# Kernel tuning notes

Hardware: AMD Instinct MI355X
Metric: run time of the kernel (lower is better)

Reference implementation:

```python
import jax, jax.numpy as jnp
import numpy as np

CHEB_K = 2  # hops per support; stacked terms = 1 + 2*CHEB_K = 5


def setup_inputs() -> dict:
    key = jax.random.key(0)
    k1, k2, k3, k4, k5 = jax.random.split(key, 5)
    B, N, C, O, D = 16, 1024, 64, 64, 10
    return {
        "x": jax.random.normal(k1, (B, N, C), dtype=jnp.float32),
        "adj": jax.random.uniform(k2, (2, B, N, N), dtype=jnp.float32),
        "node_embedding": jax.random.normal(k3, (N, D), dtype=jnp.float32),
        "weights_pool": jax.random.normal(k4, (D, 2 * CHEB_K + 1, C, O), dtype=jnp.float32) * 0.1,
        "bias_pool": jax.random.normal(k5, (D, O), dtype=jnp.float32) * 0.1,
    }


def reference(x, adj, node_embedding, weights_pool, bias_pool):
    # k-hop graph aggregation over each of the 2 supports
    out = [x]
    for s in range(adj.shape[0]):
        a = adj[s]  # [B, N, N]
        x1 = x
        for _ in range(CHEB_K):
            x1 = jnp.einsum('bnm,bmc->bnc', a, x1)
            out.append(x1)
    x_g = jnp.stack(out, axis=2)  # [B, N, K, C] with K = 2*cheb_k+1 (already node-major)
    # per-node hypernetwork weights and bias from node embeddings
    weights = jnp.einsum('nd,dkio->nkio', node_embedding, weights_pool)  # [N, K, C, O]
    bias = node_embedding @ bias_pool  # [N, O]
    # per-node contraction over (K, C)
    return jnp.einsum('bnki,nkio->bno', x_g, weights) + bias
```

## Files before the change

### kernel.cpp

```cpp
#include <hip/hip_runtime.h>
#include <stdint.h>


typedef __attribute__((ext_vector_type(4))) float f32x4;
typedef __attribute__((ext_vector_type(8))) short s16x8;
typedef __attribute__((ext_vector_type(8))) __bf16 bf16x8;

__device__ __forceinline__ unsigned short f2bf(float f) {
  union { float f; uint32_t u; } v; v.f = f;
  uint32_t r = v.u + 0x7FFFu + ((v.u >> 16) & 1u);
  return (unsigned short)(r >> 16);
}
__device__ __forceinline__ uint32_t pack2(float a, float b) {
  return (uint32_t)f2bf(a) | ((uint32_t)f2bf(b) << 16);
}

union FragU { s16x8 s; bf16x8 b; uint32_t u[4]; };

__device__ __forceinline__ void async_cp16(const void* g, void* l) {
  __builtin_amdgcn_global_load_lds(
      (const __attribute__((address_space(1))) void*)g,
      (__attribute__((address_space(3))) void*)l, 16, 0, 0);
}

__global__ __launch_bounds__(256) void cvt_adj(const float* __restrict__ adj,
                                               unsigned short* __restrict__ adjb) {
  const size_t stride = (size_t)gridDim.x * 256 * 8;
  for (size_t p = ((size_t)blockIdx.x * 256 + threadIdx.x) * 8;
       p < 33554432u; p += stride) {
    f32x4 a = *(const f32x4*)(adj + p);
    f32x4 b = *(const f32x4*)(adj + p + 4);
    union { s16x8 s; uint32_t u[4]; } o;
    o.u[0] = pack2(a[0], a[1]);
    o.u[1] = pack2(a[2], a[3]);
    o.u[2] = pack2(b[0], b[1]);
    o.u[3] = pack2(b[2], b[3]);
    *(s16x8*)(adjb + p) = o.s;
  }
}

__global__ __launch_bounds__(256) void prep(const float* __restrict__ x,
                                            const float* __restrict__ wp,
                                            unsigned short* __restrict__ XT0,
                                            unsigned short* __restrict__ X0b,
                                            unsigned short* __restrict__ wpTb) {
  __shared__ __align__(16) char smem[17160];
  const int tid = threadIdx.x;
  const int bid = blockIdx.x;
  if (bid < 256) {
    unsigned short (*tl)[72] = (unsigned short(*)[72])smem;
    const int b = bid >> 4, n0 = (bid & 15) * 64;
    {
      const int c4 = (tid & 15) * 4;
#pragma unroll
      for (int i = 0; i < 4; ++i) {
        const int row = (tid >> 4) + i * 16;
        f32x4 v =
            *(const f32x4*)(x + ((size_t)(b * 1024 + n0 + row)) * 64 + c4);
        const uint32_t w0 = pack2(v[0], v[1]);
        const uint32_t w1 = pack2(v[2], v[3]);
        *(uint32_t*)&tl[row][c4]     = w0;
        *(uint32_t*)&tl[row][c4 + 2] = w1;
        const uint64_t wq = (uint64_t)w0 | ((uint64_t)w1 << 32);
        *(uint64_t*)(X0b + ((size_t)(b * 1024 + n0 + row)) * 64 + c4) = wq;
      }
    }
    __syncthreads();
    {
      const int c = tid >> 2;
      const int nch = (tid & 3) * 16;
      s16x8 s0, s1;
#pragma unroll
      for (int j = 0; j < 8; ++j) {
        s0[j] = (short)tl[nch + j][c];
        s1[j] = (short)tl[nch + 8 + j][c];
      }
      unsigned short* p = XT0 + (size_t)(b * 64 + c) * 1024 + n0 + nch;
      *(s16x8*)p = s0;
      *(s16x8*)(p + 8) = s1;
    }
  } else {
    float (*tl)[65] = (float(*)[65])smem;
    const int jj = bid - 256;
    const int d = jj / 5, ki0 = (jj % 5) * 64;
    const float* src = wp + (size_t)d * 20480;
    {
      const int o4 = (tid & 15) * 4;
#pragma unroll
      for (int i = 0; i < 4; ++i) {
        const int row = (tid >> 4) + i * 16;
        f32x4 v = *(const f32x4*)(src + (size_t)(ki0 + row) * 64 + o4);
        tl[row][o4] = v[0]; tl[row][o4 + 1] = v[1];
        tl[row][o4 + 2] = v[2]; tl[row][o4 + 3] = v[3];
      }
    }
    __syncthreads();
    {
      const int o = tid >> 2;
      const int kch = (tid & 3) * 16;
      s16x8 s0, s1;
#pragma unroll
      for (int j = 0; j < 8; ++j) {
        s0[j] = (short)f2bf(tl[kch + j][o]);
        s1[j] = (short)f2bf(tl[kch + 8 + j][o]);
      }
      const int c0 = (ki0 + kch) >> 3;
      unsigned short* base = wpTb + (size_t)d * 24576 + (size_t)o * 384;
      *(s16x8*)(base + ((c0) ^ (o & 7)) * 8) = s0;
      *(s16x8*)(base + ((c0 + 1) ^ (o & 7)) * 8) = s1;
    }
  }
}

__device__ __forceinline__ void hop_body(
    char* smem, const unsigned short* __restrict__ A,
    const unsigned short* __restrict__ XT, unsigned short* __restrict__ Xoutb,
    unsigned short* __restrict__ XTout, int write_xt, int rowbase) {
  const int tid = threadIdx.x;
  const int wave = tid >> 6, lane = tid & 63;
  const int l15 = lane & 15, q = lane >> 4;

  unsigned short* const Ast = (unsigned short*)smem;
  unsigned short* const Bst = (unsigned short*)smem + 8192;

  const int sub = lane >> 3;
  const int ch = lane & 7;
  const unsigned short* asrc[2];
  const unsigned short* bsrc[2];
  int ldso[2];
#pragma unroll
  for (int i = 0; i < 2; ++i) {
    const int r = wave * 16 + i * 8 + sub;
    asrc[i] = A + (size_t)(rowbase + r) * 1024 + (ch ^ (r & 7)) * 8;
    bsrc[i] = XT + (size_t)r * 1024 + (ch ^ (r & 7)) * 8;
    ldso[i] = (wave * 16 + i * 8) * 64;
  }

  f32x4 acc[4];
#pragma unroll
  for (int t = 0; t < 4; ++t) acc[t] = (f32x4){0.f, 0.f, 0.f, 0.f};

  auto issue = [&](int s, int k0) {
#pragma unroll
    for (int i = 0; i < 2; ++i) {
      async_cp16(asrc[i] + k0, Ast + s * 4096 + ldso[i]);
      async_cp16(bsrc[i] + k0, Bst + s * 4096 + ldso[i]);
    }
  };
  const int sw = l15 & 7;
  auto compute = [&](int s) {
    const unsigned short* Ab = Ast + s * 4096 + (wave * 16 + l15) * 64;
    const unsigned short* Bb = Bst + s * 4096 + l15 * 64;
#pragma unroll
    for (int h = 0; h < 2; ++h) {
      const int cko = ((h * 4 + q) ^ sw) * 8;
      FragU af;
      af.s = *(const s16x8*)(Ab + cko);
#pragma unroll
      for (int t = 0; t < 4; ++t) {
        FragU bf;
        bf.s = *(const s16x8*)(Bb + t * 1024 + cko);
        acc[t] = __builtin_amdgcn_mfma_f32_16x16x32_bf16(af.b, bf.b, acc[t],
                                                         0, 0, 0);
      }
    }
  };

  issue(0, 0);
#pragma unroll 1
  for (int kt = 0; kt < 16; ++kt) {
    const int cur = kt & 1;
    __syncthreads();
    if (kt + 1 < 16) issue(cur ^ 1, (kt + 1) * 64);
    compute(cur);
  }

  __syncthreads();
  float (*tile)[65] = (float(*)[65])smem;
#pragma unroll
  for (int t = 0; t < 4; ++t)
#pragma unroll
    for (int rr = 0; rr < 4; ++rr)
      tile[wave * 16 + q * 4 + rr][t * 16 + l15] = acc[t][rr];
  __syncthreads();

  {
    const int row = tid >> 2;
    const int cb = (tid & 3) * 16;
    unsigned short* __restrict__ outp =
        Xoutb + (size_t)(rowbase + row) * 64 + cb;
    s16x8 s0, s1;
#pragma unroll
    for (int j = 0; j < 8; ++j) {
      s0[j] = (short)f2bf(tile[row][cb + j]);
      s1[j] = (short)f2bf(tile[row][cb + 8 + j]);
    }
    *(s16x8*)outp = s0;
    *(s16x8*)(outp + 8) = s1;
  }
  if (write_xt) {
    const int c = tid >> 2;
    const int nch = (tid & 3) * 16;
    unsigned short* __restrict__ xtp = XTout + (size_t)c * 1024 + rowbase + nch;
    s16x8 s0, s1;
#pragma unroll
    for (int j = 0; j < 8; ++j) {
      s0[j] = (short)f2bf(tile[nch + j][c]);
      s1[j] = (short)f2bf(tile[nch + 8 + j][c]);
    }
    *(s16x8*)xtp = s0;
    *(s16x8*)(xtp + 8) = s1;
  }
}

__global__ __launch_bounds__(256, 4) void hop1_kernel(
    const unsigned short* __restrict__ adjb,
    const unsigned short* __restrict__ XT0, unsigned short* __restrict__ X1b,
    unsigned short* __restrict__ XT1) {
  __shared__ __align__(16) char smem[32768];
  const int bx = blockIdx.x, slice = blockIdx.y, b = slice & 15;
  hop_body(smem, adjb + (size_t)slice * 1048576, XT0 + (size_t)b * 65536,
           X1b + (size_t)slice * 65536, XT1 + (size_t)slice * 65536, 1,
           bx * 64);
}

__global__ __launch_bounds__(256, 4) void hop2_kernel(
    const unsigned short* __restrict__ adjb,
    const unsigned short* __restrict__ XT1, unsigned short* __restrict__ X2b) {
  __shared__ __align__(16) char smem[32768];
  const int bx = 15 - (int)blockIdx.x;
  const int slice = 31 - (int)blockIdx.y;
  hop_body(smem, adjb + (size_t)slice * 1048576, XT1 + (size_t)slice * 65536,
           X2b + (size_t)slice * 65536, (unsigned short*)0, 0, bx * 64);
}

__global__ __launch_bounds__(512, 4) void final_kernel(
    const unsigned short* __restrict__ X0b,
    const unsigned short* __restrict__ X1b,
    const unsigned short* __restrict__ X2b,
    const unsigned short* __restrict__ wpTb, const float* __restrict__ emb,
    const float* __restrict__ bp, float* __restrict__ out) {
  __shared__ __align__(16) unsigned short wd[64][384];
  const int tid = threadIdx.x, bid = blockIdx.x;
  const int wave = tid >> 6, lane = tid & 63;
  const int l15 = lane & 15, q = lane >> 4;
  const int nd = wave >> 1, oh = wave & 1;
  const int n = bid * 4 + nd;
  const int sw2 = l15 & 7;

  FragU af10[10];
#pragma unroll
  for (int ks = 0; ks < 10; ++ks) {
    const int k = ks >> 1;
    const int cc0 = (ks & 1) * 32 + q * 8;
    const unsigned short* srcp;
    if (k == 0) {
      srcp = X0b + ((size_t)l15 * 1024 + n) * 64 + cc0;
    } else {
      const unsigned short* arr = (k == 1 || k == 3) ? X1b : X2b;
      const int s = (k >= 3) ? 1 : 0;
      srcp = arr + ((size_t)(s * 16 + l15) * 1024 + n) * 64 + cc0;
    }
    af10[ks].s = *(const s16x8*)srcp;
  }

  f32x4 acc0 = {0.f, 0.f, 0.f, 0.f}, acc1 = {0.f, 0.f, 0.f, 0.f};
  const unsigned short* wsrc = wpTb + (size_t)wave * 3072 + lane * 8;
  unsigned short* wdst = (unsigned short*)wd + wave * 3072;
#pragma unroll 1
  for (int d = 0; d < 10; ++d) {
    if (d) __syncthreads();
#pragma unroll
    for (int i = 0; i < 6; ++i)
      async_cp16(wsrc + (size_t)d * 24576 + i * 512, wdst + i * 512);
    asm volatile("s_waitcnt vmcnt(0)" ::: "memory");
    __builtin_amdgcn_sched_barrier(0);
    __syncthreads();
    f32x4 t0 = {0.f, 0.f, 0.f, 0.f}, t1 = {0.f, 0.f, 0.f, 0.f};
#pragma unroll
    for (int ks = 0; ks < 10; ++ks) {
      const int p = ((ks * 4 + q) ^ sw2) * 8;
      FragU b0, b1;
      b0.s = *(const s16x8*)&wd[oh * 32 + l15][p];
      b1.s = *(const s16x8*)&wd[oh * 32 + 16 + l15][p];
      t0 = __builtin_amdgcn_mfma_f32_16x16x32_bf16(af10[ks].b, b0.b, t0,
                                                   0, 0, 0);
      t1 = __builtin_amdgcn_mfma_f32_16x16x32_bf16(af10[ks].b, b1.b, t1,
                                                   0, 0, 0);
    }
    const float e = emb[n * 10 + d];
#pragma unroll
    for (int rr = 0; rr < 4; ++rr) {
      acc0[rr] += e * t0[rr];
      acc1[rr] += e * t1[rr];
    }
  }

#pragma unroll
  for (int tt = 0; tt < 2; ++tt) {
    const int o = oh * 32 + tt * 16 + l15;
    float bv = 0.f;
#pragma unroll
    for (int d = 0; d < 10; ++d) bv += emb[n * 10 + d] * bp[d * 64 + o];
#pragma unroll
    for (int rr = 0; rr < 4; ++rr) {
      const int bb = q * 4 + rr;
      const float a = tt ? acc1[rr] : acc0[rr];
      out[((size_t)bb * 1024 + n) * 64 + o] = a + bv;
    }
  }
}

extern "C" void kernel_launch(void* const* d_in, const int* in_sizes, int n_in,
                              void* d_out, int out_size, void* d_ws,
                              size_t ws_size, hipStream_t stream) {
  const float* x   = (const float*)d_in[0];
  const float* adj = (const float*)d_in[1];
  const float* emb = (const float*)d_in[2];
  const float* wp  = (const float*)d_in[3];
  const float* bp  = (const float*)d_in[4];
  float* out = (float*)d_out;

  char* ws = (char*)d_ws;
  unsigned short* adjb = (unsigned short*)(ws);
  unsigned short* XT0  = (unsigned short*)(ws + ((size_t)68 << 20));
  unsigned short* XT1  = (unsigned short*)(ws + ((size_t)70 << 20));
  unsigned short* X0b  = (unsigned short*)(ws + ((size_t)74 << 20));
  unsigned short* X1b  = (unsigned short*)(ws + ((size_t)76 << 20));
  unsigned short* X2b  = (unsigned short*)(ws + ((size_t)80 << 20));
  unsigned short* wpTb = (unsigned short*)(ws + ((size_t)84 << 20));

  cvt_adj<<<dim3(8192), dim3(256), 0, stream>>>(adj, adjb);
  prep<<<dim3(306), dim3(256), 0, stream>>>(x, wp, XT0, X0b, wpTb);
  hop1_kernel<<<dim3(16, 32), dim3(256), 0, stream>>>(adjb, XT0, X1b, XT1);
  hop2_kernel<<<dim3(16, 32), dim3(256), 0, stream>>>(adjb, XT1, X2b);
  final_kernel<<<dim3(256), dim3(512), 0, stream>>>(X0b, X1b, X2b, wpTb, emb,
                                                    bp, out);
}
```

Before: 259.7 us.

## Merge conversion kernels, enlarge hop tiles, read weights directly in final

The adjacency conversion and prep kernels are merged into one launch to save a launch and its tail. The hop kernels now use 512-thread blocks covering 128 rows, so each XT tile loaded into LDS is shared by twice as many adjacency rows. The final kernel drops its LDS staging of per-d weights and its block barriers, reading the unswizzled weight layout straight from global memory with smaller blocks. The costs are more LDS per block and lower occupancy in the hop kernels, and uncoalesced, cache-dependent weight reads in the final kernel.

After: 290.1 us. 1.12x slower.

```diff
diff --git a/kernel.cpp b/kernel.cpp
--- a/kernel.cpp
+++ b/kernel.cpp
@@ -23,33 +23,35 @@
       (__attribute__((address_space(3))) void*)l, 16, 0, 0);
 }
 
-__global__ __launch_bounds__(256) void cvt_adj(const float* __restrict__ adj,
-                                               unsigned short* __restrict__ adjb) {
-  const size_t stride = (size_t)gridDim.x * 256 * 8;
-  for (size_t p = ((size_t)blockIdx.x * 256 + threadIdx.x) * 8;
-       p < 33554432u; p += stride) {
-    f32x4 a = *(const f32x4*)(adj + p);
-    f32x4 b = *(const f32x4*)(adj + p + 4);
-    union { s16x8 s; uint32_t u[4]; } o;
-    o.u[0] = pack2(a[0], a[1]);
-    o.u[1] = pack2(a[2], a[3]);
-    o.u[2] = pack2(b[0], b[1]);
-    o.u[3] = pack2(b[2], b[3]);
-    *(s16x8*)(adjb + p) = o.s;
-  }
-}
-
-__global__ __launch_bounds__(256) void prep(const float* __restrict__ x,
-                                            const float* __restrict__ wp,
-                                            unsigned short* __restrict__ XT0,
-                                            unsigned short* __restrict__ X0b,
-                                            unsigned short* __restrict__ wpTb) {
+__global__ __launch_bounds__(256) void cvtprep(
+    const float* __restrict__ adj, unsigned short* __restrict__ adjb,
+    const float* __restrict__ x, const float* __restrict__ wp,
+    unsigned short* __restrict__ XT0, unsigned short* __restrict__ X0b,
+    unsigned short* __restrict__ wpTb) {
   __shared__ __align__(16) char smem[17160];
   const int tid = threadIdx.x;
   const int bid = blockIdx.x;
-  if (bid < 256) {
+
+  if (bid < 8192) {
+    const size_t stride = (size_t)8192 * 256 * 8;
+    for (size_t p = ((size_t)bid * 256 + tid) * 8; p < 33554432u;
+         p += stride) {
+      f32x4 a = *(const f32x4*)(adj + p);
+      f32x4 b = *(const f32x4*)(adj + p + 4);
+      union { s16x8 s; uint32_t u[4]; } o;
+      o.u[0] = pack2(a[0], a[1]);
+      o.u[1] = pack2(a[2], a[3]);
+      o.u[2] = pack2(b[0], b[1]);
+      o.u[3] = pack2(b[2], b[3]);
+      *(s16x8*)(adjb + p) = o.s;
+    }
+    return;
+  }
+
+  const int pid = bid - 8192;
+  if (pid < 256) {
     unsigned short (*tl)[72] = (unsigned short(*)[72])smem;
-    const int b = bid >> 4, n0 = (bid & 15) * 64;
+    const int b = pid >> 4, n0 = (pid & 15) * 64;
     {
       const int c4 = (tid & 15) * 4;
 #pragma unroll
@@ -81,7 +83,7 @@
     }
   } else {
     float (*tl)[65] = (float(*)[65])smem;
-    const int jj = bid - 256;
+    const int jj = pid - 256;
     const int d = jj / 5, ki0 = (jj % 5) * 64;
     const float* src = wp + (size_t)d * 20480;
     {
@@ -98,16 +100,16 @@
     {
       const int o = tid >> 2;
       const int kch = (tid & 3) * 16;
+      unsigned short* dst =
+          wpTb + (size_t)d * 20480 + (size_t)o * 320 + ki0 + kch;
       s16x8 s0, s1;
 #pragma unroll
       for (int j = 0; j < 8; ++j) {
         s0[j] = (short)f2bf(tl[kch + j][o]);
         s1[j] = (short)f2bf(tl[kch + 8 + j][o]);
       }
-      const int c0 = (ki0 + kch) >> 3;
-      unsigned short* base = wpTb + (size_t)d * 24576 + (size_t)o * 384;
-      *(s16x8*)(base + ((c0) ^ (o & 7)) * 8) = s0;
-      *(s16x8*)(base + ((c0 + 1) ^ (o & 7)) * 8) = s1;
+      *(s16x8*)dst = s0;
+      *(s16x8*)(dst + 8) = s1;
     }
   }
 }
@@ -121,20 +123,22 @@
   const int l15 = lane & 15, q = lane >> 4;
 
   unsigned short* const Ast = (unsigned short*)smem;
-  unsigned short* const Bst = (unsigned short*)smem + 8192;
+  unsigned short* const Bst = (unsigned short*)smem + 16384;
 
   const int sub = lane >> 3;
   const int ch = lane & 7;
   const unsigned short* asrc[2];
-  const unsigned short* bsrc[2];
-  int ldso[2];
+  int aldso[2];
 #pragma unroll
   for (int i = 0; i < 2; ++i) {
     const int r = wave * 16 + i * 8 + sub;
-    asrc[i] = A + (size_t)(rowbase + r) * 1024 + (ch ^ (r & 7)) * 8;
-    bsrc[i] = XT + (size_t)r * 1024 + (ch ^ (r & 7)) * 8;
-    ldso[i] = (wave * 16 + i * 8) * 64;
-  }
+    asrc[i] = A + (size_t)(rowbase + r) * 1024 + (ch ^ sub) * 8;
+    aldso[i] = (wave * 16 + i * 8) * 64;
+  }
+  const int rc = wave * 8 + (lane >> 3);
+  const unsigned short* bsrc =
+      XT + (size_t)rc * 1024 + ((lane & 7) ^ (rc & 7)) * 8;
+  const int bldso = wave * 512;
 
   f32x4 acc[4];
 #pragma unroll
@@ -142,14 +146,13 @@
 
   auto issue = [&](int s, int k0) {
 #pragma unroll
-    for (int i = 0; i < 2; ++i) {
-      async_cp16(asrc[i] + k0, Ast + s * 4096 + ldso[i]);
-      async_cp16(bsrc[i] + k0, Bst + s * 4096 + ldso[i]);
-    }
+    for (int i = 0; i < 2; ++i)
+      async_cp16(asrc[i] + k0, Ast + s * 8192 + aldso[i]);
+    async_cp16(bsrc + k0, Bst + s * 4096 + bldso);
   };
   const int sw = l15 & 7;
   auto compute = [&](int s) {
-    const unsigned short* Ab = Ast + s * 4096 + (wave * 16 + l15) * 64;
+    const unsigned short* Ab = Ast + s * 8192 + (wave * 16 + l15) * 64;
     const unsigned short* Bb = Bst + s * 4096 + l15 * 64;
 #pragma unroll
     for (int h = 0; h < 2; ++h) {
@@ -199,8 +202,8 @@
     *(s16x8*)(outp + 8) = s1;
   }
   if (write_xt) {
-    const int c = tid >> 2;
-    const int nch = (tid & 3) * 16;
+    const int c = tid >> 3;
+    const int nch = (tid & 7) * 16;
     unsigned short* __restrict__ xtp = XTout + (size_t)c * 1024 + rowbase + nch;
     s16x8 s0, s1;
 #pragma unroll
@@ -213,40 +216,38 @@
   }
 }
 
-__global__ __launch_bounds__(256, 4) void hop1_kernel(
+__global__ __launch_bounds__(512, 2) void hop1_kernel(
     const unsigned short* __restrict__ adjb,
     const unsigned short* __restrict__ XT0, unsigned short* __restrict__ X1b,
     unsigned short* __restrict__ XT1) {
-  __shared__ __align__(16) char smem[32768];
+  __shared__ __align__(16) char smem[49152];
   const int bx = blockIdx.x, slice = blockIdx.y, b = slice & 15;
   hop_body(smem, adjb + (size_t)slice * 1048576, XT0 + (size_t)b * 65536,
            X1b + (size_t)slice * 65536, XT1 + (size_t)slice * 65536, 1,
-           bx * 64);
-}
-
-__global__ __launch_bounds__(256, 4) void hop2_kernel(
+           bx * 128);
+}
+
+__global__ __launch_bounds__(512, 2) void hop2_kernel(
     const unsigned short* __restrict__ adjb,
     const unsigned short* __restrict__ XT1, unsigned short* __restrict__ X2b) {
-  __shared__ __align__(16) char smem[32768];
-  const int bx = 15 - (int)blockIdx.x;
+  __shared__ __align__(16) char smem[49152];
+  const int bx = 7 - (int)blockIdx.x;
   const int slice = 31 - (int)blockIdx.y;
   hop_body(smem, adjb + (size_t)slice * 1048576, XT1 + (size_t)slice * 65536,
-           X2b + (size_t)slice * 65536, (unsigned short*)0, 0, bx * 64);
-}
-
-__global__ __launch_bounds__(512, 4) void final_kernel(
+           X2b + (size_t)slice * 65536, (unsigned short*)0, 0, bx * 128);
+}
+
+__global__ __launch_bounds__(256, 2) void final_kernel(
     const unsigned short* __restrict__ X0b,
     const unsigned short* __restrict__ X1b,
     const unsigned short* __restrict__ X2b,
     const unsigned short* __restrict__ wpTb, const float* __restrict__ emb,
     const float* __restrict__ bp, float* __restrict__ out) {
-  __shared__ __align__(16) unsigned short wd[64][384];
   const int tid = threadIdx.x, bid = blockIdx.x;
   const int wave = tid >> 6, lane = tid & 63;
   const int l15 = lane & 15, q = lane >> 4;
   const int nd = wave >> 1, oh = wave & 1;
-  const int n = bid * 4 + nd;
-  const int sw2 = l15 & 7;
+  const int n = bid * 2 + nd;
 
   FragU af10[10];
 #pragma unroll
@@ -265,24 +266,16 @@
   }
 
   f32x4 acc0 = {0.f, 0.f, 0.f, 0.f}, acc1 = {0.f, 0.f, 0.f, 0.f};
-  const unsigned short* wsrc = wpTb + (size_t)wave * 3072 + lane * 8;
-  unsigned short* wdst = (unsigned short*)wd + wave * 3072;
+  const unsigned short* wb0 = wpTb + (size_t)(oh * 32 + l15) * 320 + q * 8;
 #pragma unroll 1
   for (int d = 0; d < 10; ++d) {
-    if (d) __syncthreads();
-#pragma unroll
-    for (int i = 0; i < 6; ++i)
-      async_cp16(wsrc + (size_t)d * 24576 + i * 512, wdst + i * 512);
-    asm volatile("s_waitcnt vmcnt(0)" ::: "memory");
-    __builtin_amdgcn_sched_barrier(0);
-    __syncthreads();
+    const unsigned short* wd = wb0 + (size_t)d * 20480;
     f32x4 t0 = {0.f, 0.f, 0.f, 0.f}, t1 = {0.f, 0.f, 0.f, 0.f};
 #pragma unroll
     for (int ks = 0; ks < 10; ++ks) {
-      const int p = ((ks * 4 + q) ^ sw2) * 8;
       FragU b0, b1;
-      b0.s = *(const s16x8*)&wd[oh * 32 + l15][p];
-      b1.s = *(const s16x8*)&wd[oh * 32 + 16 + l15][p];
+      b0.s = *(const s16x8*)(wd + ks * 32);
+      b1.s = *(const s16x8*)(wd + 5120 + ks * 32);
       t0 = __builtin_amdgcn_mfma_f32_16x16x32_bf16(af10[ks].b, b0.b, t0,
                                                    0, 0, 0);
       t1 = __builtin_amdgcn_mfma_f32_16x16x32_bf16(af10[ks].b, b1.b, t1,
@@ -330,10 +323,10 @@
   unsigned short* X2b  = (unsigned short*)(ws + ((size_t)80 << 20));
   unsigned short* wpTb = (unsigned short*)(ws + ((size_t)84 << 20));
 
-  cvt_adj<<<dim3(8192), dim3(256), 0, stream>>>(adj, adjb);
-  prep<<<dim3(306), dim3(256), 0, stream>>>(x, wp, XT0, X0b, wpTb);
-  hop1_kernel<<<dim3(16, 32), dim3(256), 0, stream>>>(adjb, XT0, X1b, XT1);
-  hop2_kernel<<<dim3(16, 32), dim3(256), 0, stream>>>(adjb, XT1, X2b);
-  final_kernel<<<dim3(256), dim3(512), 0, stream>>>(X0b, X1b, X2b, wpTb, emb,
+  cvtprep<<<dim3(8498), dim3(256), 0, stream>>>(adj, adjb, x, wp, XT0, X0b,
+                                                wpTb);
+  hop1_kernel<<<dim3(8, 32), dim3(512), 0, stream>>>(adjb, XT0, X1b, XT1);
+  hop2_kernel<<<dim3(8, 32), dim3(512), 0, stream>>>(adjb, XT1, X2b);
+  final_kernel<<<dim3(512), dim3(256), 0, stream>>>(X0b, X1b, X2b, wpTb, emb,
                                                     bp, out);
 }
```
